# Performance work log

Hardware: AMD Instinct MI355X
Metric: run time of the kernel (lower is better)

The kernel has to match this reference:

```python
import jax, jax.numpy as jnp
import numpy as np

ENC_DIM, DEC_DIM, ATT_DIM = 2048, 512, 512
BATCH, NPIX = 256, 196


def setup_inputs() -> dict:
    key = jax.random.key(0)
    ks = jax.random.split(key, 8)
    s = lambda d: 1.0 / np.sqrt(d)
    return {
        "encoder_out": jax.random.normal(ks[0], (BATCH, NPIX, ENC_DIM), jnp.float32),
        "decoder_hidden": jax.random.normal(ks[1], (BATCH, DEC_DIM), jnp.float32),
        "W_enc": jax.random.uniform(ks[2], (ENC_DIM, ATT_DIM), jnp.float32, -s(ENC_DIM), s(ENC_DIM)),
        "b_enc": jax.random.uniform(ks[3], (ATT_DIM,), jnp.float32, -s(ENC_DIM), s(ENC_DIM)),
        "W_dec": jax.random.uniform(ks[4], (DEC_DIM, ATT_DIM), jnp.float32, -s(DEC_DIM), s(DEC_DIM)),
        "b_dec": jax.random.uniform(ks[5], (ATT_DIM,), jnp.float32, -s(DEC_DIM), s(DEC_DIM)),
        "w_full": jax.random.uniform(ks[6], (ATT_DIM,), jnp.float32, -s(ATT_DIM), s(ATT_DIM)),
        "b_full": jax.random.uniform(ks[7], (), jnp.float32, -s(ATT_DIM), s(ATT_DIM)),
    }


def reference(encoder_out, decoder_hidden, W_enc, b_enc, W_dec, b_dec, w_full, b_full):
    # att1: (B, P, A); att2: (B, 1, A)
    att1 = jnp.einsum('bpe,ea->bpa', encoder_out, W_enc) + b_enc
    att2 = (decoder_hidden @ W_dec + b_dec)[:, None, :]
    # score: (B, P) via full_att projecting A -> 1
    att = jnp.einsum('bpa,a->bp', jax.nn.relu(att1 + att2), w_full) + b_full
    alpha = jax.nn.softmax(att, axis=1)
    context = jnp.einsum('bpe,bp->be', encoder_out, alpha)
    return context, alpha
```

## Files before the change

### kernel.cpp

```cpp
#include <hip/hip_runtime.h>
#include <hip/hip_bf16.h>

#define ENC_DIM 2048
#define DEC_DIM 512
#define ATT_DIM 512
#define BATCH   256
#define NPIX    196
#define MROWS   (BATCH * NPIX)
#define KT_N    64

typedef __attribute__((ext_vector_type(8)))  short short8;
typedef __attribute__((ext_vector_type(4)))  float f32x4;

typedef const __attribute__((address_space(1))) unsigned int gu32;
typedef __attribute__((address_space(3))) unsigned int lu32;

__device__ __forceinline__ short f2bf(float x) {
    unsigned u = __builtin_bit_cast(unsigned, x);
    unsigned r = (u + 0x7FFFu + ((u >> 16) & 1u)) >> 16;
    return (short)r;
}
__device__ __forceinline__ unsigned pkbf(float a, float b) {
    unsigned r;
    asm("v_cvt_pk_bf16_f32 %0, %1, %2" : "=v"(r) : "v"(a), "v"(b));
    return r;
}

__global__ __launch_bounds__(256) void bahdanau_prep(
    const float* __restrict__ dec_h, const float* __restrict__ W_enc,
    const float* __restrict__ b_enc, const float* __restrict__ W_dec,
    const float* __restrict__ b_dec,
    float* __restrict__ att2pb, short* __restrict__ Wpack)
{
    int blk = blockIdx.x;
    if (blk < BATCH) {
        __shared__ float hs[DEC_DIM];
        int b = blk;
        for (int i = threadIdx.x; i < DEC_DIM; i += 256) hs[i] = dec_h[b * DEC_DIM + i];
        __syncthreads();
        for (int a = threadIdx.x; a < ATT_DIM; a += 256) {
            float s = 0.f;
            #pragma unroll 8
            for (int d = 0; d < DEC_DIM; ++d) s += hs[d] * W_dec[d * ATT_DIM + a];
            att2pb[b * ATT_DIM + a] = s + b_dec[a] + b_enc[a];
        }
    } else {
        int c  = (blk - BATCH) * 256 + threadIdx.x;
        int l  = c & 63;
        int kt = (c >> 6) & 63;
        int nt = c >> 12;
        int n     = nt * 16 + (l & 15);
        int kbase = kt * 32 + ((l >> 4) & 3) * 8;
        short8 v;
        #pragma unroll
        for (int j = 0; j < 8; ++j) v[j] = f2bf(W_enc[(kbase + j) * ATT_DIM + n]);
        *reinterpret_cast<short8*>(Wpack + (size_t)c * 8) = v;
    }
}

__global__ __launch_bounds__(256) void bahdanau_gemm(
    const float* __restrict__ enc, const float* __restrict__ w_full,
    const float* __restrict__ att2pb, const short* __restrict__ Wpack,
    float* __restrict__ spart)
{
    __shared__ __align__(16) char lds[2 * 24576];
    __shared__ float redm[2][128];

    const int wg = blockIdx.x;
    const int mt = ((wg >> 5) << 3) | (wg & 7);
    const int nc = (wg >> 3) & 3;

    const int tid  = threadIdx.x;
    const int lane = tid & 63;
    const int wid  = tid >> 6;
    const int wm   = wid >> 1;
    const int wn   = wid & 1;

    size_t aoff[4];
    #pragma unroll
    for (int s = 0; s < 4; ++s) {
        int i = tid + 256 * s, r = i >> 3, qq = i & 7;
        aoff[s] = (size_t)(mt * 128 + r) * ENC_DIM + ((qq ^ (r & 7)) << 2);
    }
    size_t boff[2];
    #pragma unroll
    for (int s = 0; s < 2; ++s) {
        int i = tid + 256 * s, f = i >> 6, ln = i & 63;
        boff[s] = ((size_t)(nc * 8 + f) * 64 * 64 + ln) * 8;
    }

    f32x4 acc[4][4];
    #pragma unroll
    for (int a = 0; a < 4; ++a)
        #pragma unroll
        for (int c = 0; c < 4; ++c)
            #pragma unroll
            for (int r = 0; r < 4; ++r) acc[a][c][r] = 0.f;

    auto STAGE = [&](int buf, int kt) {
        char* ab = lds + buf * 24576;
        char* bb = ab + 16384;
        #pragma unroll
        for (int s = 0; s < 4; ++s)
            __builtin_amdgcn_global_load_lds((gu32*)(enc + aoff[s] + kt * 32),
                                             (lu32*)(ab + (tid + 256 * s) * 16), 16, 0, 0);
        #pragma unroll
        for (int s = 0; s < 2; ++s)
            __builtin_amdgcn_global_load_lds((gu32*)(Wpack + boff[s] + (size_t)kt * 512),
                                             (lu32*)(bb + (tid + 256 * s) * 16), 16, 0, 0);
    };

    auto COMPUTE = [&](int buf) {
        const char* ab = lds + buf * 24576;
        const char* bb = ab + 16384;
        short8 af[4], bf[4];
        #pragma unroll
        for (int rt = 0; rt < 4; ++rt) {
            int r  = wm * 64 + rt * 16 + (lane & 15);
            int q0 = ((lane >> 4) & 3) * 2;
            float4 lo = *reinterpret_cast<const float4*>(ab + r * 128 + ((q0       ^ (r & 7)) << 4));
            float4 hi = *reinterpret_cast<const float4*>(ab + r * 128 + (((q0 + 1) ^ (r & 7)) << 4));
            union { short8 s; unsigned u[4]; } fr;
            fr.u[0] = pkbf(lo.x, lo.y); fr.u[1] = pkbf(lo.z, lo.w);
            fr.u[2] = pkbf(hi.x, hi.y); fr.u[3] = pkbf(hi.z, hi.w);
            af[rt] = fr.s;
        }
        #pragma unroll
        for (int ct = 0; ct < 4; ++ct)
            bf[ct] = *reinterpret_cast<const short8*>(bb + (wn * 4 + ct) * 1024 + lane * 16);
        #pragma unroll
        for (int rt = 0; rt < 4; ++rt)
            #pragma unroll
            for (int ct = 0; ct < 4; ++ct)
                acc[rt][ct] = __builtin_amdgcn_mfma_f32_16x16x32_bf16(af[rt], bf[ct], acc[rt][ct], 0, 0, 0);
    };

    STAGE(0, 0);
    __syncthreads();
    for (int kt2 = 0; kt2 < KT_N; kt2 += 2) {
        STAGE(1, kt2 + 1);
        COMPUTE(0);
        __syncthreads();
        if (kt2 + 2 < KT_N) STAGE(0, kt2 + 2);
        COMPUTE(1);
        __syncthreads();
    }

    float srow[16];
    #pragma unroll
    for (int i = 0; i < 16; ++i) srow[i] = 0.f;
    #pragma unroll
    for (int ct = 0; ct < 4; ++ct) {
        int col  = nc * 128 + wn * 64 + ct * 16 + (lane & 15);
        float wf = w_full[col];
        #pragma unroll
        for (int rt = 0; rt < 4; ++rt) {
            #pragma unroll
            for (int r = 0; r < 4; ++r) {
                unsigned grow = mt * 128 + wm * 64 + rt * 16 + ((lane >> 4) & 3) * 4 + r;
                unsigned bb   = grow / NPIX;
                float v = acc[rt][ct][r] + att2pb[bb * ATT_DIM + col];
                srow[rt * 4 + r] += fmaxf(v, 0.f) * wf;
            }
        }
    }
    #pragma unroll
    for (int i = 0; i < 16; ++i) {
        float v = srow[i];
        v += __shfl_xor(v, 1);
        v += __shfl_xor(v, 2);
        v += __shfl_xor(v, 4);
        v += __shfl_xor(v, 8);
        srow[i] = v;
    }
    if ((lane & 15) == 0) {
        #pragma unroll
        for (int rt = 0; rt < 4; ++rt)
            #pragma unroll
            for (int r = 0; r < 4; ++r)
                redm[wn][wm * 64 + rt * 16 + ((lane >> 4) & 3) * 4 + r] = srow[rt * 4 + r];
    }
    __syncthreads();
    if (tid < 128)
        spart[(size_t)nc * MROWS + mt * 128 + tid] = redm[0][tid] + redm[1][tid];
}

__global__ __launch_bounds__(512) void bahdanau_ctx(
    const float* __restrict__ enc, const float* __restrict__ spart,
    float* __restrict__ out_ctx, float* __restrict__ out_alpha)
{
    __shared__ float al[256];
    __shared__ float msum[2];
    const int b    = blockIdx.x;
    const int tid  = threadIdx.x;
    const int lane = tid & 63;
    const int wid  = tid >> 6;

    if (tid < NPIX) {
        int row = b * NPIX + tid;
        al[tid] = spart[row] + spart[MROWS + row] + spart[2 * MROWS + row] + spart[3 * MROWS + row];
    } else if (tid < 256) {
        al[tid] = -3.4e38f;
    }
    __syncthreads();

    if (wid == 0) {
        float s0 = al[lane], s1 = al[lane + 64], s2 = al[lane + 128], s3 = al[lane + 192];
        float m = fmaxf(fmaxf(s0, s1), fmaxf(s2, s3));
        #pragma unroll
        for (int d = 1; d <= 32; d <<= 1) m = fmaxf(m, __shfl_xor(m, d));
        float e = __expf(s0 - m) + __expf(s1 - m) + __expf(s2 - m) + __expf(s3 - m);
        #pragma unroll
        for (int d = 1; d <= 32; d <<= 1) e += __shfl_xor(e, d);
        if (lane == 0) { msum[0] = m; msum[1] = e; }
    }
    __syncthreads();
    float m    = msum[0];
    float rinv = 1.f / msum[1];
    if (tid < NPIX) {
        float a = __expf(al[tid] - m) * rinv;
        al[tid] = a;
        out_alpha[b * NPIX + tid] = a;
    }
    __syncthreads();

    float4 c4 = {0.f, 0.f, 0.f, 0.f};
    const float4* enc4 = reinterpret_cast<const float4*>(enc + (size_t)b * NPIX * ENC_DIM);
    #pragma unroll 4
    for (int p = 0; p < NPIX; ++p) {
        float a  = al[p];
        float4 v = enc4[(size_t)p * (ENC_DIM / 4) + tid];
        c4.x += a * v.x; c4.y += a * v.y; c4.z += a * v.z; c4.w += a * v.w;
    }
    reinterpret_cast<float4*>(out_ctx)[(size_t)b * (ENC_DIM / 4) + tid] = c4;
}

extern "C" void kernel_launch(void* const* d_in, const int* in_sizes, int n_in,
                              void* d_out, int out_size, void* d_ws, size_t ws_size,
                              hipStream_t stream) {
    const float* enc    = (const float*)d_in[0];
    const float* dech   = (const float*)d_in[1];
    const float* W_enc  = (const float*)d_in[2];
    const float* b_enc  = (const float*)d_in[3];
    const float* W_dec  = (const float*)d_in[4];
    const float* b_dec  = (const float*)d_in[5];
    const float* w_full = (const float*)d_in[6];

    float* att2pb = (float*)d_ws;
    short* Wpack  = (short*)((char*)d_ws + 512 * 1024);
    float* spart  = (float*)((char*)d_ws + 2560 * 1024);

    float* out_ctx   = (float*)d_out;
    float* out_alpha = out_ctx + (size_t)BATCH * ENC_DIM;

    bahdanau_prep<<<768, 256, 0, stream>>>(dech, W_enc, b_enc, W_dec, b_dec, att2pb, Wpack);
    bahdanau_gemm<<<1568, 256, 0, stream>>>(enc, w_full, att2pb, Wpack, spart);
    bahdanau_ctx<<<BATCH, 512, 0, stream>>>(enc, spart, out_ctx, out_alpha);
}
```

Before: 425.8 us.

## Triple-buffer GEMM LDS pipeline with vmcnt waits and fragment-ordered A layout

Replaces the double-buffered K loop with a three-stage LDS ring, using explicit s_waitcnt vmcnt counts and raw barriers so two tiles of global loads stay in flight while one is computed. The A tile is now written to LDS in MFMA-fragment order, so each lane reads contiguous 16-byte chunks without the XOR swizzle. Launch bounds request two blocks per CU. LDS use grows to about 72KB per block, which may limit occupancy, and the hand-counted waits are fragile.

```diff
diff --git a/kernel.cpp b/kernel.cpp
--- a/kernel.cpp
+++ b/kernel.cpp
@@ -8,6 +8,7 @@
 #define NPIX    196
 #define MROWS   (BATCH * NPIX)
 #define KT_N    64
+#define BUFSZ   24576
 
 typedef __attribute__((ext_vector_type(8)))  short short8;
 typedef __attribute__((ext_vector_type(4)))  float f32x4;
@@ -58,12 +59,12 @@
     }
 }
 
-__global__ __launch_bounds__(256) void bahdanau_gemm(
+__global__ __launch_bounds__(256, 2) void bahdanau_gemm(
     const float* __restrict__ enc, const float* __restrict__ w_full,
     const float* __restrict__ att2pb, const short* __restrict__ Wpack,
     float* __restrict__ spart)
 {
-    __shared__ __align__(16) char lds[2 * 24576];
+    __shared__ __align__(16) char lds[3 * BUFSZ];
     __shared__ float redm[2][128];
 
     const int wg = blockIdx.x;
@@ -79,14 +80,17 @@
     size_t aoff[4];
     #pragma unroll
     for (int s = 0; s < 4; ++s) {
-        int i = tid + 256 * s, r = i >> 3, qq = i & 7;
-        aoff[s] = (size_t)(mt * 128 + r) * ENC_DIM + ((qq ^ (r & 7)) << 2);
+        int ca = tid + 256 * s;
+        int l = ca & 63, h = (ca >> 6) & 1, rt = ca >> 7;
+        aoff[s] = (size_t)(mt * 128 + rt * 16 + (l & 15)) * ENC_DIM
+                + ((l >> 4) & 3) * 8 + h * 4;
     }
     size_t boff[2];
     #pragma unroll
     for (int s = 0; s < 2; ++s) {
-        int i = tid + 256 * s, f = i >> 6, ln = i & 63;
-        boff[s] = ((size_t)(nc * 8 + f) * 64 * 64 + ln) * 8;
+        int cb = tid + 256 * s;
+        int f = cb >> 6, l = cb & 63;
+        boff[s] = (size_t)(nc * 8 + f) * 32768 + (size_t)l * 8;
     }
 
     f32x4 acc[4][4];
@@ -97,54 +101,67 @@
             #pragma unroll
             for (int r = 0; r < 4; ++r) acc[a][c][r] = 0.f;
 
-    auto STAGE = [&](int buf, int kt) {
-        char* ab = lds + buf * 24576;
-        char* bb = ab + 16384;
+    auto STAGE = [&](char* base, int kt) {
         #pragma unroll
         for (int s = 0; s < 4; ++s)
             __builtin_amdgcn_global_load_lds((gu32*)(enc + aoff[s] + kt * 32),
-                                             (lu32*)(ab + (tid + 256 * s) * 16), 16, 0, 0);
+                                             (lu32*)(base + (tid + 256 * s) * 16), 16, 0, 0);
         #pragma unroll
         for (int s = 0; s < 2; ++s)
             __builtin_amdgcn_global_load_lds((gu32*)(Wpack + boff[s] + (size_t)kt * 512),
-                                             (lu32*)(bb + (tid + 256 * s) * 16), 16, 0, 0);
+                                             (lu32*)(base + 16384 + (tid + 256 * s) * 16), 16, 0, 0);
     };
 
-    auto COMPUTE = [&](int buf) {
-        const char* ab = lds + buf * 24576;
-        const char* bb = ab + 16384;
+    auto COMPUTE = [&](const char* base) {
         short8 af[4], bf[4];
         #pragma unroll
-        for (int rt = 0; rt < 4; ++rt) {
-            int r  = wm * 64 + rt * 16 + (lane & 15);
-            int q0 = ((lane >> 4) & 3) * 2;
-            float4 lo = *reinterpret_cast<const float4*>(ab + r * 128 + ((q0       ^ (r & 7)) << 4));
-            float4 hi = *reinterpret_cast<const float4*>(ab + r * 128 + (((q0 + 1) ^ (r & 7)) << 4));
+        for (int rw = 0; rw < 4; ++rw) {
+            int rt = wm * 4 + rw;
+            float4 lo = *reinterpret_cast<const float4*>(base + ((rt * 2 + 0) * 64 + lane) * 16);
+            float4 hi = *reinterpret_cast<const float4*>(base + ((rt * 2 + 1) * 64 + lane) * 16);
             union { short8 s; unsigned u[4]; } fr;
             fr.u[0] = pkbf(lo.x, lo.y); fr.u[1] = pkbf(lo.z, lo.w);
             fr.u[2] = pkbf(hi.x, hi.y); fr.u[3] = pkbf(hi.z, hi.w);
-            af[rt] = fr.s;
+            af[rw] = fr.s;
         }
         #pragma unroll
         for (int ct = 0; ct < 4; ++ct)
-            bf[ct] = *reinterpret_cast<const short8*>(bb + (wn * 4 + ct) * 1024 + lane * 16);
-        #pragma unroll
-        for (int rt = 0; rt < 4; ++rt)
+            bf[ct] = *reinterpret_cast<const short8*>(base + 16384 + ((wn * 4 + ct) * 64 + lane) * 16);
+        #pragma unroll
+        for (int rw = 0; rw < 4; ++rw)
             #pragma unroll
             for (int ct = 0; ct < 4; ++ct)
-                acc[rt][ct] = __builtin_amdgcn_mfma_f32_16x16x32_bf16(af[rt], bf[ct], acc[rt][ct], 0, 0, 0);
+                acc[rw][ct] = __builtin_amdgcn_mfma_f32_16x16x32_bf16(af[rw], bf[ct], acc[rw][ct], 0, 0, 0);
     };
 
-    STAGE(0, 0);
-    __syncthreads();
-    for (int kt2 = 0; kt2 < KT_N; kt2 += 2) {
-        STAGE(1, kt2 + 1);
-        COMPUTE(0);
-        __syncthreads();
-        if (kt2 + 2 < KT_N) STAGE(0, kt2 + 2);
-        COMPUTE(1);
-        __syncthreads();
-    }
+    char* p0 = lds;
+    char* p1 = lds + BUFSZ;
+    char* p2 = lds + 2 * BUFSZ;
+
+    STAGE(p0, 0);
+    STAGE(p1, 1);
+    STAGE(p2, 2);
+
+    for (int t = 0; t < KT_N - 3; ++t) {
+        asm volatile("s_waitcnt vmcnt(12)" ::: "memory");
+        __builtin_amdgcn_s_barrier();
+        COMPUTE(p0);
+        asm volatile("s_waitcnt lgkmcnt(0)" ::: "memory");
+        __builtin_amdgcn_s_barrier();
+        STAGE(p0, t + 3);
+        char* tmp = p0; p0 = p1; p1 = p2; p2 = tmp;
+    }
+    asm volatile("s_waitcnt vmcnt(12)" ::: "memory");
+    __builtin_amdgcn_s_barrier();
+    COMPUTE(p0);
+    { char* tmp = p0; p0 = p1; p1 = p2; p2 = tmp; }
+    asm volatile("s_waitcnt vmcnt(6)" ::: "memory");
+    __builtin_amdgcn_s_barrier();
+    COMPUTE(p0);
+    { char* tmp = p0; p0 = p1; p1 = p2; p2 = tmp; }
+    asm volatile("s_waitcnt vmcnt(0)" ::: "memory");
+    __builtin_amdgcn_s_barrier();
+    COMPUTE(p0);
 
     float srow[16];
     #pragma unroll
@@ -157,7 +174,7 @@
         for (int rt = 0; rt < 4; ++rt) {
             #pragma unroll
             for (int r = 0; r < 4; ++r) {
-                unsigned grow = mt * 128 + wm * 64 + rt * 16 + ((lane >> 4) & 3) * 4 + r;
+                unsigned grow = mt * 128 + wm * 64 + rt * 16 + (lane >> 4) * 4 + r;
                 unsigned bb   = grow / NPIX;
                 float v = acc[rt][ct][r] + att2pb[bb * ATT_DIM + col];
                 srow[rt * 4 + r] += fmaxf(v, 0.f) * wf;
@@ -178,7 +195,7 @@
         for (int rt = 0; rt < 4; ++rt)
             #pragma unroll
             for (int r = 0; r < 4; ++r)
-                redm[wn][wm * 64 + rt * 16 + ((lane >> 4) & 3) * 4 + r] = srow[rt * 4 + r];
+                redm[wn][wm * 64 + rt * 16 + (lane >> 4) * 4 + r] = srow[rt * 4 + r];
     }
     __syncthreads();
     if (tid < 128)
```

Measured after the change: 430.4 us. No clear change (+1.1%).
